# Optimization experiments

Measured on AMD Instinct MI355X. Metric: run time of the kernel, lower is better.

The kernel has to match this reference:

```python
import jax, jax.numpy as jnp
import numpy as np

C = 64  # channel dim fixed by Conv1D filters=64 and residual add

def setup_inputs() -> dict:
    key = jax.random.key(0)
    kF, kM, kN, kV = jax.random.split(key, 4)
    B, T = 8, 2048
    F = jax.random.normal(kF, (B, T, C), dtype=jnp.float32)
    # Conv1D(kernel_size=1, use_bias=False) == pointwise dense: weight [C_in, filters]
    scale = 1.0 / np.sqrt(C)
    W_M = jax.random.normal(kM, (C, C), dtype=jnp.float32) * scale
    W_N = jax.random.normal(kN, (C, C), dtype=jnp.float32) * scale
    W_V = jax.random.normal(kV, (C, C), dtype=jnp.float32) * scale
    return {"F": F, "W_M": W_M, "W_N": W_N, "W_V": W_V}

def reference(F, W_M, W_N, W_V):
    # 1x1 conv projections (pointwise matmul over channel dim)
    M = jnp.einsum('btc,cd->btd', F, W_M)  # Q
    N = jnp.einsum('btc,cd->btd', F, W_N)  # K
    V = jnp.einsum('btc,cd->btd', F, W_V)
    # correlation = Q @ K^T ; softmax over last axis (keras Softmax default)
    scores = jnp.einsum('bqd,bkd->bqk', M, N)  # [B, T, T]
    S = jax.nn.softmax(scores, axis=-1)
    out = jnp.einsum('bqk,bkd->bqd', S, V)
    return out + F  # residual
```

## Files before the change

### kernel.cpp

```cpp
#include <hip/hip_runtime.h>
#include <hip/hip_bf16.h>

#define B_ 8
#define T_ 2048
#define LOG2E 1.4426950408889634f

typedef _Float16 half8 __attribute__((ext_vector_type(8)));
typedef _Float16 half4 __attribute__((ext_vector_type(4)));
typedef float f32x4 __attribute__((ext_vector_type(4)));

#define MFMA16(A, Bv, Cv) __builtin_amdgcn_mfma_f32_16x16x32_f16((A), (Bv), (Cv), 0, 0, 0)

__device__ inline float xexp2(float x)
{
    float r;
    asm("v_exp_f32 %0, %1" : "=v"(r) : "v"(x));
    return r;
}

__global__ __launch_bounds__(256) void proj_kernel(
    const float* __restrict__ F, const float* __restrict__ WM,
    const float* __restrict__ WN, const float* __restrict__ WV,
    _Float16* __restrict__ Qf, _Float16* __restrict__ Kf,
    _Float16* __restrict__ Vf)
{
    const int lane = threadIdx.x & 63;
    const int dt   = threadIdx.x >> 6;
    const int ql = lane & 15;
    const int g  = lane >> 4;
    const int blk = blockIdx.x;
    const int b   = blk & 7;
    const int rt  = blk >> 3;
    const int rowbase = b * T_ + rt * 16;
    const int d = dt * 16 + ql;

    const float* fr = F + (size_t)(rowbase + ql) * 64;
    const f32x4 v00 = *(const f32x4*)(fr + 8 * g);
    const f32x4 v01 = *(const f32x4*)(fr + 8 * g + 4);
    const f32x4 v10 = *(const f32x4*)(fr + 32 + 8 * g);
    const f32x4 v11 = *(const f32x4*)(fr + 32 + 8 * g + 4);
    half8 af0, af1;
#pragma unroll
    for (int j = 0; j < 4; ++j) {
        af0[j]     = (_Float16)v00[j];
        af0[4 + j] = (_Float16)v01[j];
        af1[j]     = (_Float16)v10[j];
        af1[4 + j] = (_Float16)v11[j];
    }

    half8 wq0, wq1, wk0, wk1, wv0, wv1;
#pragma unroll
    for (int j = 0; j < 8; ++j) {
        const int k0 = (8 * g + j) * 64 + d;
        const int k1 = (32 + 8 * g + j) * 64 + d;
        wq0[j] = (_Float16)WM[k0];
        wq1[j] = (_Float16)WM[k1];
        wk0[j] = (_Float16)WN[k0];
        wk1[j] = (_Float16)WN[k1];
        wv0[j] = (_Float16)WV[k0];
        wv1[j] = (_Float16)WV[k1];
    }

    f32x4 z = {0.f, 0.f, 0.f, 0.f};
    f32x4 accQ = MFMA16(wq0, af0, z);
    accQ = MFMA16(wq1, af1, accQ);
    f32x4 accK = MFMA16(wk0, af0, z);
    accK = MFMA16(wk1, af1, accK);
    f32x4 accV = MFMA16(af0, wv0, z);
    accV = MFMA16(af1, wv1, accV);

    const int d0 = dt * 16 + 4 * g;
    const int p  = ((d0 >> 5) << 2) | ((d0 >> 3) & 3);
    const size_t tbase = (((size_t)b * 128 + rt) * 8 + p) * 128 + ql * 8 + (d0 & 7);
    {
        half4 qs;
#pragma unroll
        for (int r = 0; r < 4; ++r) qs[r] = (_Float16)(accQ[r] * LOG2E);
        *(half4*)(Qf + tbase) = qs;
    }
    {
        half4 ks;
#pragma unroll
        for (int r = 0; r < 4; ++r) ks[r] = (_Float16)accK[r];
        *(half4*)(Kf + tbase) = ks;
    }
    {
        half4 vs;
#pragma unroll
        for (int r = 0; r < 4; ++r) vs[r] = (_Float16)accV[r];
        const int kt5 = rt >> 1;
        const int cp0 = 8 * g + 4 * (rt & 1);
        *(half4*)(Vf + ((((size_t)b * 64 + kt5) * 4 + dt) * 16 + ql) * 32 + cp0) = vs;
    }
}

#define PMAX(s0, s1)                                                         \
    fmaxf(fmaxf(fmaxf(fmaxf(s0[0], s0[1]), s0[2]),                           \
                fmaxf(fmaxf(s0[3], s1[0]), s1[1])),                          \
          fmaxf(s1[2], s1[3]))

#define RESC(pm, mr, ls, a0, a1, a2, a3)                                     \
    do {                                                                     \
        float pmw = fmaxf(pm, __shfl_xor(pm, 16));                           \
        pmw = fmaxf(pmw, __shfl_xor(pmw, 32));                               \
        const float mnew = fmaxf(mr, pmw);                                   \
        const float fac  = xexp2(mr - mnew);                                 \
        mr = mnew;                                                           \
        ls *= fac;                                                           \
        const int lg = 4 * ((threadIdx.x & 63) >> 4);                        \
        const int lb = (threadIdx.x & 48);                                   \
        const float f0 = __shfl(fac, lb | (lg + 0));                         \
        const float f1 = __shfl(fac, lb | (lg + 1));                         \
        const float f2 = __shfl(fac, lb | (lg + 2));                         \
        const float f3 = __shfl(fac, lb | (lg + 3));                         \
        a0[0] *= f0; a0[1] *= f1; a0[2] *= f2; a0[3] *= f3;                  \
        a1[0] *= f0; a1[1] *= f1; a1[2] *= f2; a1[3] *= f3;                  \
        a2[0] *= f0; a2[1] *= f1; a2[2] *= f2; a2[3] *= f3;                  \
        a3[0] *= f0; a3[1] *= f1; a3[2] *= f2; a3[3] *= f3;                  \
    } while (0)

#define EXPPACK(s0, s1, mr, ls, pav)                                         \
    do {                                                                     \
        const float e0 = xexp2(s0[0] - mr), e1 = xexp2(s0[1] - mr);          \
        const float e2 = xexp2(s0[2] - mr), e3 = xexp2(s0[3] - mr);          \
        const float e4 = xexp2(s1[0] - mr), e5 = xexp2(s1[1] - mr);          \
        const float e6 = xexp2(s1[2] - mr), e7 = xexp2(s1[3] - mr);          \
        ls += ((e0 + e1) + (e2 + e3)) + ((e4 + e5) + (e6 + e7));             \
        pav[0] = (_Float16)e0; pav[1] = (_Float16)e1;                        \
        pav[2] = (_Float16)e2; pav[3] = (_Float16)e3;                        \
        pav[4] = (_Float16)e4; pav[5] = (_Float16)e5;                        \
        pav[6] = (_Float16)e6; pav[7] = (_Float16)e7;                        \
    } while (0)

__global__ __launch_bounds__(512, 1) void attn_kernel(
    const _Float16* __restrict__ Qf, const _Float16* __restrict__ Kf,
    const _Float16* __restrict__ Vf, const float* __restrict__ F,
    float* __restrict__ out)
{
    __shared__ float Ol[8][64][68];
    __shared__ float Ml[8][64];
    __shared__ float Ll[8][64];

    const int lane = threadIdx.x & 63;
    const int wid  = threadIdx.x >> 6;
    const int blk  = blockIdx.x;
    const int b    = blk & 7;
    const int tile = blk >> 3;
    const int ql = lane & 15;
    const int g  = lane >> 4;

    const half8* QfB = (const half8*)Qf + (size_t)b * 16384;
    const half8* KfB = (const half8*)Kf + (size_t)b * 16384;
    const half8* VfB = (const half8*)Vf + (size_t)b * 16384;

    const half8* qtA = QfB + (size_t)(4 * tile + 0) * 128;
    const half8* qtB = QfB + (size_t)(4 * tile + 1) * 128;
    const half8* qtC = QfB + (size_t)(4 * tile + 2) * 128;
    const half8* qtD = QfB + (size_t)(4 * tile + 3) * 128;
    const half8 qA0 = qtA[g * 16 + ql], qA1 = qtA[(4 + g) * 16 + ql];
    const half8 qB0 = qtB[g * 16 + ql], qB1 = qtB[(4 + g) * 16 + ql];
    const half8 qC0 = qtC[g * 16 + ql], qC1 = qtC[(4 + g) * 16 + ql];
    const half8 qD0 = qtD[g * 16 + ql], qD1 = qtD[(4 + g) * 16 + ql];

    const f32x4 z4 = {0.f, 0.f, 0.f, 0.f};
    f32x4 aA0 = z4, aA1 = z4, aA2 = z4, aA3 = z4;
    f32x4 aB0 = z4, aB1 = z4, aB2 = z4, aB3 = z4;
    f32x4 aC0 = z4, aC1 = z4, aC2 = z4, aC3 = z4;
    f32x4 aD0 = z4, aD1 = z4, aD2 = z4, aD3 = z4;
    float mA = -1e30f, lsA = 0.f;
    float mB = -1e30f, lsB = 0.f;
    float mC = -1e30f, lsC = 0.f;
    float mD = -1e30f, lsD = 0.f;

    const int kb0 = wid << 8;
    const half8* kA = KfB + (size_t)(kb0 >> 4) * 128 + g * 16 + ql;
    const half8* vA = VfB + (size_t)(kb0 >> 5) * 256 + ql * 4 + g;

    half8 k0lo = kA[0];
    half8 k0hi = kA[64];
    half8 k1lo = kA[128];
    half8 k1hi = kA[192];
    half8 v0 = vA[0];
    half8 v1 = vA[64];
    half8 v2 = vA[128];
    half8 v3 = vA[192];

    for (int it = 0; it < 8; ++it) {
        half8 nk0lo, nk0hi, nk1lo, nk1hi, nv0, nv1, nv2, nv3;
        if (it < 7) {
            nk0lo = kA[256];
            nk0hi = kA[256 + 64];
            nk1lo = kA[256 + 128];
            nk1hi = kA[256 + 192];
            nv0 = vA[256];
            nv1 = vA[256 + 64];
            nv2 = vA[256 + 128];
            nv3 = vA[256 + 192];
        }

        f32x4 sA0 = z4, sA1 = z4, sB0 = z4, sB1 = z4;
        f32x4 sC0 = z4, sC1 = z4, sD0 = z4, sD1 = z4;
        sA0 = MFMA16(k0lo, qA0, sA0);
        sB0 = MFMA16(k0lo, qB0, sB0);
        sC0 = MFMA16(k0lo, qC0, sC0);
        sD0 = MFMA16(k0lo, qD0, sD0);
        sA1 = MFMA16(k1lo, qA0, sA1);
        sB1 = MFMA16(k1lo, qB0, sB1);
        sC1 = MFMA16(k1lo, qC0, sC1);
        sD1 = MFMA16(k1lo, qD0, sD1);
        sA0 = MFMA16(k0hi, qA1, sA0);
        sB0 = MFMA16(k0hi, qB1, sB0);
        sC0 = MFMA16(k0hi, qC1, sC0);
        sD0 = MFMA16(k0hi, qD1, sD0);
        sA1 = MFMA16(k1hi, qA1, sA1);
        sB1 = MFMA16(k1hi, qB1, sB1);
        sC1 = MFMA16(k1hi, qC1, sC1);
        sD1 = MFMA16(k1hi, qD1, sD1);

        const float pmA = PMAX(sA0, sA1);
        const float pmB = PMAX(sB0, sB1);
        const float pmC = PMAX(sC0, sC1);
        const float pmD = PMAX(sD0, sD1);
        const float trig = fmaxf(fmaxf(pmA - mA, pmB - mB),
                                 fmaxf(pmC - mC, pmD - mD));
        if (__any(trig > 8.0f)) {
            RESC(pmA, mA, lsA, aA0, aA1, aA2, aA3);
            RESC(pmB, mB, lsB, aB0, aB1, aB2, aB3);
            RESC(pmC, mC, lsC, aC0, aC1, aC2, aC3);
            RESC(pmD, mD, lsD, aD0, aD1, aD2, aD3);
        }

        half8 pavA, pavB, pavC, pavD;
        EXPPACK(sA0, sA1, mA, lsA, pavA);
        EXPPACK(sB0, sB1, mB, lsB, pavB);
        EXPPACK(sC0, sC1, mC, lsC, pavC);
        EXPPACK(sD0, sD1, mD, lsD, pavD);

        aA0 = MFMA16(pavA, v0, aA0);
        aB0 = MFMA16(pavB, v0, aB0);
        aC0 = MFMA16(pavC, v0, aC0);
        aD0 = MFMA16(pavD, v0, aD0);
        aA1 = MFMA16(pavA, v1, aA1);
        aB1 = MFMA16(pavB, v1, aB1);
        aC1 = MFMA16(pavC, v1, aC1);
        aD1 = MFMA16(pavD, v1, aD1);
        aA2 = MFMA16(pavA, v2, aA2);
        aB2 = MFMA16(pavB, v2, aB2);
        aC2 = MFMA16(pavC, v2, aC2);
        aD2 = MFMA16(pavD, v2, aD2);
        aA3 = MFMA16(pavA, v3, aA3);
        aB3 = MFMA16(pavB, v3, aB3);
        aC3 = MFMA16(pavC, v3, aC3);
        aD3 = MFMA16(pavD, v3, aD3);

        if (it < 7) {
            k0lo = nk0lo; k0hi = nk0hi; k1lo = nk1lo; k1hi = nk1hi;
            v0 = nv0; v1 = nv1; v2 = nv2; v3 = nv3;
        }
        kA += 256;
        vA += 256;
    }

    lsA += __shfl_xor(lsA, 16); lsA += __shfl_xor(lsA, 32);
    lsB += __shfl_xor(lsB, 16); lsB += __shfl_xor(lsB, 32);
    lsC += __shfl_xor(lsC, 16); lsC += __shfl_xor(lsC, 32);
    lsD += __shfl_xor(lsD, 16); lsD += __shfl_xor(lsD, 32);

#pragma unroll
    for (int r = 0; r < 4; ++r) {
        Ol[wid][     4 * g + r][ 0 + ql] = aA0[r];
        Ol[wid][     4 * g + r][16 + ql] = aA1[r];
        Ol[wid][     4 * g + r][32 + ql] = aA2[r];
        Ol[wid][     4 * g + r][48 + ql] = aA3[r];
        Ol[wid][16 + 4 * g + r][ 0 + ql] = aB0[r];
        Ol[wid][16 + 4 * g + r][16 + ql] = aB1[r];
        Ol[wid][16 + 4 * g + r][32 + ql] = aB2[r];
        Ol[wid][16 + 4 * g + r][48 + ql] = aB3[r];
        Ol[wid][32 + 4 * g + r][ 0 + ql] = aC0[r];
        Ol[wid][32 + 4 * g + r][16 + ql] = aC1[r];
        Ol[wid][32 + 4 * g + r][32 + ql] = aC2[r];
        Ol[wid][32 + 4 * g + r][48 + ql] = aC3[r];
        Ol[wid][48 + 4 * g + r][ 0 + ql] = aD0[r];
        Ol[wid][48 + 4 * g + r][16 + ql] = aD1[r];
        Ol[wid][48 + 4 * g + r][32 + ql] = aD2[r];
        Ol[wid][48 + 4 * g + r][48 + ql] = aD3[r];
    }
    if (g == 0) {
        Ml[wid][     ql] = mA;  Ll[wid][     ql] = lsA;
        Ml[wid][16 + ql] = mB;  Ll[wid][16 + ql] = lsB;
        Ml[wid][32 + ql] = mC;  Ll[wid][32 + ql] = lsC;
        Ml[wid][48 + ql] = mD;  Ll[wid][48 + ql] = lsD;
    }
    __syncthreads();

    const int tid = threadIdx.x;
    const int qq  = tid >> 3;
    const int d0  = (tid & 7) * 8;

    float mm[8], lv[8];
#pragma unroll
    for (int s = 0; s < 8; ++s) {
        mm[s] = Ml[s][qq];
        lv[s] = Ll[s][qq];
    }
    float ms = mm[0];
#pragma unroll
    for (int s = 1; s < 8; ++s) ms = fmaxf(ms, mm[s]);
    float lt = 0.f;
    f32x4 oa = {0.f, 0.f, 0.f, 0.f};
    f32x4 ob2 = {0.f, 0.f, 0.f, 0.f};
#pragma unroll
    for (int s = 0; s < 8; ++s) {
        const float sc = xexp2(mm[s] - ms);
        lt += lv[s] * sc;
        oa  += *(const f32x4*)(&Ol[s][qq][d0])     * sc;
        ob2 += *(const f32x4*)(&Ol[s][qq][d0 + 4]) * sc;
    }
    const float inv = 1.0f / lt;
    const size_t grow = (size_t)b * T_ + (tile << 6) + qq;
    const f32x4 fr0 = *(const f32x4*)(F + grow * 64 + d0);
    const f32x4 fr1 = *(const f32x4*)(F + grow * 64 + d0 + 4);
    *(f32x4*)(out + grow * 64 + d0)     = oa * inv + fr0;
    *(f32x4*)(out + grow * 64 + d0 + 4) = ob2 * inv + fr1;
}

extern "C" void kernel_launch(void* const* d_in, const int* in_sizes, int n_in,
                              void* d_out, int out_size, void* d_ws, size_t ws_size,
                              hipStream_t stream)
{
    const float* F  = (const float*)d_in[0];
    const float* WM = (const float*)d_in[1];
    const float* WN = (const float*)d_in[2];
    const float* WV = (const float*)d_in[3];
    float* out = (float*)d_out;

    const size_t proj_bytes = (size_t)B_ * T_ * 64 * sizeof(_Float16);
    char* ws = (char*)d_ws;
    _Float16* Qf = (_Float16*)(ws);
    _Float16* Kf = (_Float16*)(ws + proj_bytes);
    _Float16* Vf = (_Float16*)(ws + 2 * proj_bytes);

    hipLaunchKernelGGL(proj_kernel, dim3(B_ * T_ / 16), dim3(256), 0, stream,
                       F, WM, WN, WV, Qf, Kf, Vf);
    hipLaunchKernelGGL(attn_kernel, dim3(B_ * T_ / 64), dim3(512), 0, stream,
                       Qf, Kf, Vf, F, out);
}
```

Measured before the change: 26.67 us.

## Compute softmax row sums via MFMA with ones vector; halve projection grid

The attention kernel drops the per-lane scalar accumulation of exponentials and the cross-lane reductions. Row sums now come from an extra MFMA against an all-ones B operand, which lands them in the same layout as the output accumulators and folds them into the rescale path. This trades VALU adds and shuffles for four extra MFMAs per iteration and more accumulator registers. Separately, the projection kernel processes two row tiles per block, so converted weights are reused and the grid is halved.

```diff
diff --git a/kernel.cpp b/kernel.cpp
--- a/kernel.cpp
+++ b/kernel.cpp
@@ -30,23 +30,8 @@
     const int g  = lane >> 4;
     const int blk = blockIdx.x;
     const int b   = blk & 7;
-    const int rt  = blk >> 3;
-    const int rowbase = b * T_ + rt * 16;
+    const int rt0 = (blk >> 3) * 2;
     const int d = dt * 16 + ql;
-
-    const float* fr = F + (size_t)(rowbase + ql) * 64;
-    const f32x4 v00 = *(const f32x4*)(fr + 8 * g);
-    const f32x4 v01 = *(const f32x4*)(fr + 8 * g + 4);
-    const f32x4 v10 = *(const f32x4*)(fr + 32 + 8 * g);
-    const f32x4 v11 = *(const f32x4*)(fr + 32 + 8 * g + 4);
-    half8 af0, af1;
-#pragma unroll
-    for (int j = 0; j < 4; ++j) {
-        af0[j]     = (_Float16)v00[j];
-        af0[4 + j] = (_Float16)v01[j];
-        af1[j]     = (_Float16)v10[j];
-        af1[4 + j] = (_Float16)v11[j];
-    }
 
     half8 wq0, wq1, wk0, wk1, wv0, wv1;
 #pragma unroll
@@ -61,36 +46,57 @@
         wv1[j] = (_Float16)WV[k1];
     }
 
-    f32x4 z = {0.f, 0.f, 0.f, 0.f};
-    f32x4 accQ = MFMA16(wq0, af0, z);
-    accQ = MFMA16(wq1, af1, accQ);
-    f32x4 accK = MFMA16(wk0, af0, z);
-    accK = MFMA16(wk1, af1, accK);
-    f32x4 accV = MFMA16(af0, wv0, z);
-    accV = MFMA16(af1, wv1, accV);
-
-    const int d0 = dt * 16 + 4 * g;
-    const int p  = ((d0 >> 5) << 2) | ((d0 >> 3) & 3);
-    const size_t tbase = (((size_t)b * 128 + rt) * 8 + p) * 128 + ql * 8 + (d0 & 7);
-    {
-        half4 qs;
-#pragma unroll
-        for (int r = 0; r < 4; ++r) qs[r] = (_Float16)(accQ[r] * LOG2E);
-        *(half4*)(Qf + tbase) = qs;
-    }
-    {
-        half4 ks;
-#pragma unroll
-        for (int r = 0; r < 4; ++r) ks[r] = (_Float16)accK[r];
-        *(half4*)(Kf + tbase) = ks;
-    }
-    {
-        half4 vs;
-#pragma unroll
-        for (int r = 0; r < 4; ++r) vs[r] = (_Float16)accV[r];
-        const int kt5 = rt >> 1;
-        const int cp0 = 8 * g + 4 * (rt & 1);
-        *(half4*)(Vf + ((((size_t)b * 64 + kt5) * 4 + dt) * 16 + ql) * 32 + cp0) = vs;
+#pragma unroll 2
+    for (int rr = 0; rr < 2; ++rr) {
+        const int rt = rt0 + rr;
+        const int rowbase = b * T_ + rt * 16;
+
+        const float* fr = F + (size_t)(rowbase + ql) * 64;
+        const f32x4 v00 = *(const f32x4*)(fr + 8 * g);
+        const f32x4 v01 = *(const f32x4*)(fr + 8 * g + 4);
+        const f32x4 v10 = *(const f32x4*)(fr + 32 + 8 * g);
+        const f32x4 v11 = *(const f32x4*)(fr + 32 + 8 * g + 4);
+        half8 af0, af1;
+#pragma unroll
+        for (int j = 0; j < 4; ++j) {
+            af0[j]     = (_Float16)v00[j];
+            af0[4 + j] = (_Float16)v01[j];
+            af1[j]     = (_Float16)v10[j];
+            af1[4 + j] = (_Float16)v11[j];
+        }
+
+        f32x4 z = {0.f, 0.f, 0.f, 0.f};
+        f32x4 accQ = MFMA16(wq0, af0, z);
+        accQ = MFMA16(wq1, af1, accQ);
+        f32x4 accK = MFMA16(wk0, af0, z);
+        accK = MFMA16(wk1, af1, accK);
+        f32x4 accV = MFMA16(af0, wv0, z);
+        accV = MFMA16(af1, wv1, accV);
+
+        const int d0 = dt * 16 + 4 * g;
+        const int p  = ((d0 >> 5) << 2) | ((d0 >> 3) & 3);
+        const size_t tbase =
+            (((size_t)b * 128 + rt) * 8 + p) * 128 + ql * 8 + (d0 & 7);
+        {
+            half4 qs;
+#pragma unroll
+            for (int r = 0; r < 4; ++r) qs[r] = (_Float16)(accQ[r] * LOG2E);
+            *(half4*)(Qf + tbase) = qs;
+        }
+        {
+            half4 ks;
+#pragma unroll
+            for (int r = 0; r < 4; ++r) ks[r] = (_Float16)accK[r];
+            *(half4*)(Kf + tbase) = ks;
+        }
+        {
+            half4 vs;
+#pragma unroll
+            for (int r = 0; r < 4; ++r) vs[r] = (_Float16)accV[r];
+            const int kt5 = rt >> 1;
+            const int cp0 = 8 * g + 4 * (rt & 1);
+            *(half4*)(Vf + ((((size_t)b * 64 + kt5) * 4 + dt) * 16 + ql) * 32 + cp0) = vs;
+        }
     }
 }
 
@@ -99,14 +105,13 @@
                 fmaxf(fmaxf(s0[3], s1[0]), s1[1])),                          \
           fmaxf(s1[2], s1[3]))
 
-#define RESC(pm, mr, ls, a0, a1, a2, a3)                                     \
+#define RESC(pm, mr, a0, a1, a2, a3, a4)                                     \
     do {                                                                     \
         float pmw = fmaxf(pm, __shfl_xor(pm, 16));                           \
         pmw = fmaxf(pmw, __shfl_xor(pmw, 32));                               \
         const float mnew = fmaxf(mr, pmw);                                   \
         const float fac  = xexp2(mr - mnew);                                 \
         mr = mnew;                                                           \
-        ls *= fac;                                                           \
         const int lg = 4 * ((threadIdx.x & 63) >> 4);                        \
         const int lb = (threadIdx.x & 48);                                   \
         const float f0 = __shfl(fac, lb | (lg + 0));                         \
@@ -117,15 +122,15 @@
         a1[0] *= f0; a1[1] *= f1; a1[2] *= f2; a1[3] *= f3;                  \
         a2[0] *= f0; a2[1] *= f1; a2[2] *= f2; a2[3] *= f3;                  \
         a3[0] *= f0; a3[1] *= f1; a3[2] *= f2; a3[3] *= f3;                  \
+        a4[0] *= f0; a4[1] *= f1; a4[2] *= f2; a4[3] *= f3;                  \
     } while (0)
 
-#define EXPPACK(s0, s1, mr, ls, pav)                                         \
+#define EXPPACK(s0, s1, mr, pav)                                             \
     do {                                                                     \
         const float e0 = xexp2(s0[0] - mr), e1 = xexp2(s0[1] - mr);          \
         const float e2 = xexp2(s0[2] - mr), e3 = xexp2(s0[3] - mr);          \
         const float e4 = xexp2(s1[0] - mr), e5 = xexp2(s1[1] - mr);          \
         const float e6 = xexp2(s1[2] - mr), e7 = xexp2(s1[3] - mr);          \
-        ls += ((e0 + e1) + (e2 + e3)) + ((e4 + e5) + (e6 + e7));             \
         pav[0] = (_Float16)e0; pav[1] = (_Float16)e1;                        \
         pav[2] = (_Float16)e2; pav[3] = (_Float16)e3;                        \
         pav[4] = (_Float16)e4; pav[5] = (_Float16)e5;                        \
@@ -162,15 +167,16 @@
     const half8 qC0 = qtC[g * 16 + ql], qC1 = qtC[(4 + g) * 16 + ql];
     const half8 qD0 = qtD[g * 16 + ql], qD1 = qtD[(4 + g) * 16 + ql];
 
+    half8 vone;
+#pragma unroll
+    for (int j = 0; j < 8; ++j) vone[j] = (_Float16)1.0f;
+
     const f32x4 z4 = {0.f, 0.f, 0.f, 0.f};
-    f32x4 aA0 = z4, aA1 = z4, aA2 = z4, aA3 = z4;
-    f32x4 aB0 = z4, aB1 = z4, aB2 = z4, aB3 = z4;
-    f32x4 aC0 = z4, aC1 = z4, aC2 = z4, aC3 = z4;
-    f32x4 aD0 = z4, aD1 = z4, aD2 = z4, aD3 = z4;
-    float mA = -1e30f, lsA = 0.f;
-    float mB = -1e30f, lsB = 0.f;
-    float mC = -1e30f, lsC = 0.f;
-    float mD = -1e30f, lsD = 0.f;
+    f32x4 aA0 = z4, aA1 = z4, aA2 = z4, aA3 = z4, aA4 = z4;
+    f32x4 aB0 = z4, aB1 = z4, aB2 = z4, aB3 = z4, aB4 = z4;
+    f32x4 aC0 = z4, aC1 = z4, aC2 = z4, aC3 = z4, aC4 = z4;
+    f32x4 aD0 = z4, aD1 = z4, aD2 = z4, aD3 = z4, aD4 = z4;
+    float mA = -1e30f, mB = -1e30f, mC = -1e30f, mD = -1e30f;
 
     const int kb0 = wid << 8;
     const half8* kA = KfB + (size_t)(kb0 >> 4) * 128 + g * 16 + ql;
@@ -224,17 +230,17 @@
         const float trig = fmaxf(fmaxf(pmA - mA, pmB - mB),
                                  fmaxf(pmC - mC, pmD - mD));
         if (__any(trig > 8.0f)) {
-            RESC(pmA, mA, lsA, aA0, aA1, aA2, aA3);
-            RESC(pmB, mB, lsB, aB0, aB1, aB2, aB3);
-            RESC(pmC, mC, lsC, aC0, aC1, aC2, aC3);
-            RESC(pmD, mD, lsD, aD0, aD1, aD2, aD3);
+            RESC(pmA, mA, aA0, aA1, aA2, aA3, aA4);
+            RESC(pmB, mB, aB0, aB1, aB2, aB3, aB4);
+            RESC(pmC, mC, aC0, aC1, aC2, aC3, aC4);
+            RESC(pmD, mD, aD0, aD1, aD2, aD3, aD4);
         }
 
         half8 pavA, pavB, pavC, pavD;
-        EXPPACK(sA0, sA1, mA, lsA, pavA);
-        EXPPACK(sB0, sB1, mB, lsB, pavB);
-        EXPPACK(sC0, sC1, mC, lsC, pavC);
-        EXPPACK(sD0, sD1, mD, lsD, pavD);
+        EXPPACK(sA0, sA1, mA, pavA);
+        EXPPACK(sB0, sB1, mB, pavB);
+        EXPPACK(sC0, sC1, mC, pavC);
+        EXPPACK(sD0, sD1, mD, pavD);
 
         aA0 = MFMA16(pavA, v0, aA0);
         aB0 = MFMA16(pavB, v0, aB0);
@@ -252,6 +258,10 @@
         aB3 = MFMA16(pavB, v3, aB3);
         aC3 = MFMA16(pavC, v3, aC3);
         aD3 = MFMA16(pavD, v3, aD3);
+        aA4 = MFMA16(pavA, vone, aA4);
+        aB4 = MFMA16(pavB, vone, aB4);
+        aC4 = MFMA16(pavC, vone, aC4);
+        aD4 = MFMA16(pavD, vone, aD4);
 
         if (it < 7) {
             k0lo = nk0lo; k0hi = nk0hi; k1lo = nk1lo; k1hi = nk1hi;
@@ -260,11 +270,6 @@
         kA += 256;
         vA += 256;
     }
-
-    lsA += __shfl_xor(lsA, 16); lsA += __shfl_xor(lsA, 32);
-    lsB += __shfl_xor(lsB, 16); lsB += __shfl_xor(lsB, 32);
-    lsC += __shfl_xor(lsC, 16); lsC += __shfl_xor(lsC, 32);
-    lsD += __shfl_xor(lsD, 16); lsD += __shfl_xor(lsD, 32);
 
 #pragma unroll
     for (int r = 0; r < 4; ++r) {
@@ -286,10 +291,19 @@
         Ol[wid][48 + 4 * g + r][48 + ql] = aD3[r];
     }
     if (g == 0) {
-        Ml[wid][     ql] = mA;  Ll[wid][     ql] = lsA;
-        Ml[wid][16 + ql] = mB;  Ll[wid][16 + ql] = lsB;
-        Ml[wid][32 + ql] = mC;  Ll[wid][32 + ql] = lsC;
-        Ml[wid][48 + ql] = mD;  Ll[wid][48 + ql] = lsD;
+        Ml[wid][     ql] = mA;
+        Ml[wid][16 + ql] = mB;
+        Ml[wid][32 + ql] = mC;
+        Ml[wid][48 + ql] = mD;
+    }
+    if (ql == 0) {
+#pragma unroll
+        for (int r = 0; r < 4; ++r) {
+            Ll[wid][     4 * g + r] = aA4[r];
+            Ll[wid][16 + 4 * g + r] = aB4[r];
+            Ll[wid][32 + 4 * g + r] = aC4[r];
+            Ll[wid][48 + 4 * g + r] = aD4[r];
+        }
     }
     __syncthreads();
 
@@ -340,7 +354,7 @@
     _Float16* Kf = (_Float16*)(ws + proj_bytes);
     _Float16* Vf = (_Float16*)(ws + 2 * proj_bytes);
 
-    hipLaunchKernelGGL(proj_kernel, dim3(B_ * T_ / 16), dim3(256), 0, stream,
+    hipLaunchKernelGGL(proj_kernel, dim3(B_ * T_ / 32), dim3(256), 0, stream,
                        F, WM, WN, WV, Qf, Kf, Vf);
     hipLaunchKernelGGL(attn_kernel, dim3(B_ * T_ / 64), dim3(512), 0, stream,
                        Qf, Kf, Vf, F, out);
```

Result: no change. 26.22 us (-1.7%).
